# Optimization experiments

Hardware: AMD Instinct MI355X
Metric: run time of the kernel (lower is better)

## Reference

```python
import jax, jax.numpy as jnp
import numpy as np

UNITS = 128
INPUT_DIM = 784
OUTPUT_DIM = 10
NUM_LAYERS = 8
BATCH = 2048
DT = 0.1
EPS = 0.01
TOL = 1e-4
STEPS = 15


def setup_inputs() -> dict:
    key = jax.random.key(0)
    k = jax.random.split(key, 7)
    s_in = 1.0 / np.sqrt(INPUT_DIM)
    s_u = 1.0 / np.sqrt(UNITS)
    return {
        "x": jax.random.normal(k[0], (BATCH, INPUT_DIM), jnp.float32),
        "w_in": jax.random.uniform(k[1], (UNITS, INPUT_DIM), jnp.float32, -s_in, s_in),
        "b_in": jax.random.uniform(k[2], (UNITS,), jnp.float32, -s_in, s_in),
        "w_blocks": jax.random.uniform(k[3], (NUM_LAYERS, UNITS, UNITS), jnp.float32, -s_u, s_u),
        "b_blocks": jax.random.uniform(k[4], (NUM_LAYERS, UNITS), jnp.float32, -s_u, s_u),
        "w_out": jax.random.uniform(k[5], (OUTPUT_DIM, UNITS), jnp.float32, -s_u, s_u),
        "b_out": jax.random.uniform(k[6], (OUTPUT_DIM,), jnp.float32, -s_u, s_u),
    }


def _build_A(w_blocks):
    # A_l = [[I, dt*W_l], [-dt*W_l^T, (1+dt/eps)*I]], shape [L, 2u, 2u]
    I = jnp.broadcast_to(jnp.eye(UNITS, dtype=w_blocks.dtype), (NUM_LAYERS, UNITS, UNITS))
    top = jnp.concatenate([I, DT * w_blocks], axis=2)
    bot = jnp.concatenate([-DT * jnp.transpose(w_blocks, (0, 2, 1)), (1.0 + DT / EPS) * I], axis=2)
    return jnp.concatenate([top, bot], axis=1)


def _sweep(z_in, A, b_blocks):
    # Fixed-point sweeping (no-grad region in the original). z_ls: [L, B, 2u]
    B = z_in.shape[0]

    def layer_step(z, xs):
        A_l, b_l, z_l = xs
        rhs = jnp.concatenate(
            [jnp.broadcast_to(DT * b_l, (B, UNITS)), (DT / EPS) * jnp.tanh(z_l[:, :UNITS])],
            axis=1,
        ) + z
        # A_l is shared across the batch: one LU, many rhs
        y = jnp.linalg.solve(A_l, rhs.T).T
        err = jnp.mean(jnp.linalg.norm(z_l - y, axis=1))
        return y, (y, err)

    def body(state):
        z_ls, _, step = state
        _, (new_zls, errs) = jax.lax.scan(layer_step, z_in, (A, b_blocks, z_ls))
        return (new_zls, jnp.mean(errs), step + 1)

    def cond(state):
        _, err, step = state
        return jnp.logical_and(step < STEPS, err > TOL)

    z0 = jnp.broadcast_to(z_in[None], (NUM_LAYERS,) + z_in.shape)
    z_ls, _, _ = jax.lax.while_loop(cond, body, (z0, jnp.float32(10.0), jnp.int32(0)))
    return z_ls


def _block(z_in, W, b, z_l):
    # implicit_forward of one TransNetLayerSweeping (z_l is the converged sweep state)
    u_l, v_l = z_l[:, :UNITS], z_l[:, UNITS:]
    u_out = -DT * (v_l @ W.T) + z_in[:, :UNITS] + DT * b
    v_out = DT * (u_l @ W) + z_in[:, UNITS:] - (DT / EPS) * (v_l - jnp.tanh(u_l))
    return jnp.concatenate([u_out, v_out], axis=1)


def reference(x, w_in, b_in, w_blocks, b_blocks, w_out, b_out):
    x1 = x @ w_in.T + b_in                                  # [B, u]
    z_in = jnp.concatenate([x1, jnp.tanh(x1)], axis=1)      # [B, 2u]
    z_ls = _sweep(z_in, _build_A(w_blocks), b_blocks)       # [L, B, 2u]
    # Original loop does z = block.implicit_forward(z_in) for every block,
    # so only the LAST block's output survives.
    z_out = _block(z_in, w_blocks[-1], b_blocks[-1], z_ls[-1])
    logits = z_out[:, :UNITS] @ w_out.T + b_out             # [B, out]
    return jax.nn.softmax(logits, axis=1)
```

## Files before the change

### kernel.cpp

```cpp
#include <hip/hip_runtime.h>

#define U 128
#define BATCH 2048
#define NL 8
#define NS 8
#define DTc 0.1f
#define TENf 10.0f
#define INVC (1.0f/11.0f)
#define AFACT (0.01f/11.0f)
#define AST 264

typedef unsigned short u16;
typedef __attribute__((ext_vector_type(8))) short bf16x8;
typedef __attribute__((ext_vector_type(4))) float f32x4;
#define MFMA16(a,b,c) __builtin_amdgcn_mfma_f32_16x16x32_bf16(a,b,c,0,0,0)

__device__ __forceinline__ float bf2f(u16 h){ return __uint_as_float(((unsigned int)h)<<16); }
__device__ __forceinline__ u16 f2bf(float f){
  unsigned int u = __float_as_uint(f);
  u += 0x7FFFu + ((u >> 16) & 1u);
  return (u16)(u >> 16);
}
__device__ __forceinline__ float fast_tanh(float x){
  float e = __expf(2.0f*x);
  return 1.0f - __fdividef(2.0f, e + 1.0f);
}
__device__ __forceinline__ int detect_md(const u16* x, int* s_bad, int t, int nthr){
  if(t==0) *s_bad = 0;
  __syncthreads();
  int f=0;
  for(int i=t;i<4096;i+=nthr){ float v = bf2f(x[i]); if(!(fabsf(v)<16.0f)) f=1; }
  if(f) atomicOr(s_bad,1);
  __syncthreads();
  return *s_bad ? 0 : 1;
}

__global__ __launch_bounds__(256) void convK(
    const void* __restrict__ xraw, const void* __restrict__ w_in,
    const void* __restrict__ b_in, const void* __restrict__ wb,
    const void* __restrict__ bb, const void* __restrict__ w_out,
    const void* __restrict__ b_out,
    u16* __restrict__ winb, u16* __restrict__ Wg, u16* __restrict__ Wtg,
    float* __restrict__ bbD, float* __restrict__ b_in_f,
    float* __restrict__ w_out_f, float* __restrict__ b_out_f){
  __shared__ int s_bad;
  const int t = threadIdx.x;
  const int md = detect_md((const u16*)xraw, &s_bad, t, 256);
  const int g = blockIdx.x*256 + t, GS = gridDim.x*256;
  for(int i=g;i<100352;i+=GS) winb[i] = md ? ((const u16*)w_in)[i] : f2bf(((const float*)w_in)[i]);
  for(int i=g;i<131072;i+=GS){
    u16 h = md ? ((const u16*)wb)[i] : f2bf(((const float*)wb)[i]);
    Wg[i] = h;
    int L = i>>14, j = i & 16383;
    Wtg[(L<<14) + (j&127)*U + (j>>7)] = h;
  }
  for(int i=g;i<NL*U;i+=GS) bbD[i] = DTc * (md ? bf2f(((const u16*)bb)[i]) : ((const float*)bb)[i]);
  for(int i=g;i<U;i+=GS)    b_in_f[i]  = md ? bf2f(((const u16*)b_in)[i])  : ((const float*)b_in)[i];
  for(int i=g;i<1280;i+=GS) w_out_f[i] = md ? bf2f(((const u16*)w_out)[i]) : ((const float*)w_out)[i];
  for(int i=g;i<10;i+=GS)   b_out_f[i] = md ? bf2f(((const u16*)b_out)[i]) : ((const float*)b_out)[i];
}

template<typename EPI>
__device__ __forceinline__ void tile16(const u16* __restrict__ A, int lda,
                                       const u16* __restrict__ B, int ldb, EPI epi){
  const int lane = threadIdx.x & 63, w = threadIdx.x >> 6;
  const int ln = lane & 15, lq = lane >> 4;
  const int n0 = 32*w + ln, n1 = n0 + 16;
  bf16x8 af[4], b0[4], b1[4];
  #pragma unroll
  for(int kt=0;kt<4;kt++){
    af[kt] = *(const bf16x8*)&A[ln*lda + kt*32 + lq*8];
    b0[kt] = *(const bf16x8*)&B[n0*ldb + kt*32 + lq*8];
    b1[kt] = *(const bf16x8*)&B[n1*ldb + kt*32 + lq*8];
  }
  f32x4 a0 = {0,0,0,0}, a1 = {0,0,0,0};
  #pragma unroll
  for(int kt=0;kt<4;kt++){ a0 = MFMA16(af[kt], b0[kt], a0); a1 = MFMA16(af[kt], b1[kt], a1); }
  epi(a0, a1, n0, n1);
}

__global__ __launch_bounds__(256) void gemmP(const u16* __restrict__ Wtg, u16* __restrict__ Pg){
  const int L = blockIdx.x >> 3, mt = blockIdx.x & 7;
  const int lq = (threadIdx.x & 63) >> 4;
  const u16* WtL = Wtg + (L<<14);
  tile16(WtL + mt*16*U, U, WtL, U, [&](f32x4 a0, f32x4 a1, int n0, int n1){
    #pragma unroll
    for(int r=0;r<4;r++){
      int row = mt*16 + lq*4 + r;
      Pg[(L<<14) + row*U + n0] = f2bf(AFACT*a0[r]);
      Pg[(L<<14) + row*U + n1] = f2bf(AFACT*a1[r]);
    }
  });
}
__global__ __launch_bounds__(256) void gemmS(const u16* __restrict__ Pg, u16* __restrict__ Fb){
  const int L = blockIdx.x >> 3, mt = blockIdx.x & 7;
  const int lq = (threadIdx.x & 63) >> 4;
  const u16* PL = Pg + (L<<14);
  u16* FbL = Fb + (size_t)L*65536;
  tile16(PL + mt*16*U, U, PL, U, [&](f32x4 a0, f32x4 a1, int n0, int n1){
    #pragma unroll
    for(int r=0;r<4;r++){
      int row = mt*16 + lq*4 + r;
      FbL[row*256 + n0] = f2bf(INVC*(((row==n0)?1.0f:0.0f) - bf2f(PL[row*U+n0]) + a0[r]));
      FbL[row*256 + n1] = f2bf(INVC*(((row==n1)?1.0f:0.0f) - bf2f(PL[row*U+n1]) + a1[r]));
    }
  });
}
__global__ __launch_bounds__(256) void gemmQ(const u16* __restrict__ Fb, const u16* __restrict__ Wg,
                                             u16* __restrict__ FbW){
  const int L = blockIdx.x >> 3, mt = blockIdx.x & 7;
  const int lq = (threadIdx.x & 63) >> 4;
  const u16* FbL = Fb + (size_t)L*65536;
  u16* FbO = FbW + (size_t)L*65536;
  tile16(FbL + mt*16*256, 256, Wg + (L<<14), U, [&](f32x4 a0, f32x4 a1, int n0, int n1){
    #pragma unroll
    for(int r=0;r<4;r++){
      int row = mt*16 + lq*4 + r;
      u16 q0 = f2bf(DTc*a0[r]), q1 = f2bf(DTc*a1[r]);
      FbO[row*256 + 128 + n0] = q0;
      FbO[row*256 + 128 + n1] = q1;
      FbO[(128+n0)*256 + row] = q0;
      FbO[(128+n1)*256 + row] = q1;
    }
  });
}
__global__ __launch_bounds__(256) void gemmR(const u16* __restrict__ Wg, u16* __restrict__ Fb){
  const int L = blockIdx.x >> 3, mt = blockIdx.x & 7;
  const int lq = (threadIdx.x & 63) >> 4;
  u16* FbL = Fb + (size_t)L*65536;
  tile16(Wg + (L<<14) + mt*16*U, U, FbL + 128*256, 256, [&](f32x4 a0, f32x4 a1, int n0, int n1){
    #pragma unroll
    for(int r=0;r<4;r++){
      int row = mt*16 + lq*4 + r;
      FbL[(128+row)*256 + 128 + n0] = f2bf(DTc*a0[r]);
      FbL[(128+row)*256 + 128 + n1] = f2bf(DTc*a1[r]);
    }
  });
}
__global__ __launch_bounds__(256) void swizK(const u16* __restrict__ Fb, u16* __restrict__ Fsw){
  const int L = blockIdx.x >> 3, part = blockIdx.x & 7;
  const u16* FbL = Fb + (size_t)L*65536;
  for(int i = part*1024 + threadIdx.x; i < (part+1)*1024; i += 256){
    int lanei = i & 63, kt = (i>>6)&7, c = (i>>9)&3, w = (i>>11)&3;
    int lni = lanei & 15, lqi = lanei >> 4;
    int row_n = 64*w + 16*c + lni;
    int col_k = kt*32 + lqi*8;
    *(bf16x8*)&Fsw[((size_t)L*8192 + i)*8] = *(const bf16x8*)&FbL[row_n*256 + col_k];
  }
}

__global__ __launch_bounds__(512,1) void mainK(
    const void* __restrict__ xraw, const u16* __restrict__ winb,
    const float* __restrict__ b_in_f, const bf16x8* __restrict__ Fsw,
    const float* __restrict__ bbD, const float* __restrict__ w_out_f,
    const float* __restrict__ b_out_f, void* __restrict__ outraw){
  __shared__ u16 At[2][16*AST];
  __shared__ unsigned zh32[NL][16][64];
  __shared__ float zinu[16*U];
  __shared__ float bbL[NL*U];
  __shared__ float lg[16*12];
  __shared__ int s_bad;
  float* uout = (float*)&At[0][0];

  const int t = threadIdx.x;
  const int lane = t & 63, wid = t >> 6, ln = lane & 15, lq = lane >> 4;
  const int r0 = blockIdx.x * 16;

  const int md = detect_md((const u16*)xraw, &s_bad, t, 512);
  for(int i=t;i<NL*U;i+=512) bbL[i] = bbD[i];
  __syncthreads();

  {
    const int n0 = 16*wid + ln;
    f32x4 acc = {0,0,0,0};
    for(int kt=0; kt<25; ++kt){
      int k0 = kt*32 + lq*8;
      bf16x8 av = {0,0,0,0,0,0,0,0}, bv = {0,0,0,0,0,0,0,0};
      if(k0 < 784){
        if(md){
          av = *(const bf16x8*)((const u16*)xraw + (size_t)(r0+ln)*784 + k0);
        } else {
          const float* xp = (const float*)xraw + (size_t)(r0+ln)*784 + k0;
          float4 f0 = *(const float4*)xp, f1 = *(const float4*)(xp+4);
          av[0]=(short)f2bf(f0.x); av[1]=(short)f2bf(f0.y); av[2]=(short)f2bf(f0.z); av[3]=(short)f2bf(f0.w);
          av[4]=(short)f2bf(f1.x); av[5]=(short)f2bf(f1.y); av[6]=(short)f2bf(f1.z); av[7]=(short)f2bf(f1.w);
        }
        bv = *(const bf16x8*)&winb[(size_t)n0*784 + k0];
      }
      acc = MFMA16(av, bv, acc);
    }
    #pragma unroll
    for(int r=0;r<4;r++) zinu[(lq*4+r)*U + n0] = acc[r] + b_in_f[n0];
  }
  __syncthreads();

  for(int i=t; i<NL*16*64; i+=512){
    int l = i>>10, row = (i>>6)&15, p = i & 63;
    int lo = 32*(p>>4) + (p&15);
    zh32[l][row][p] = ((unsigned)f2bf(zinu[row*U + lo + 16]) << 16) | f2bf(zinu[row*U + lo]);
  }
  float ru[2][4];
  if(wid < 4){
    #pragma unroll
    for(int cc=0;cc<2;cc++){
      int n = 32*wid + 16*cc + ln;
      #pragma unroll
      for(int r=0;r<4;r++){
        int row = lq*4 + r;
        At[0][row*AST + n] = f2bf((TENf + 1.0f) * fast_tanh(zinu[row*U + n]));
      }
    }
  } else {
    int w4 = wid - 4;
    #pragma unroll
    for(int cc=0;cc<2;cc++){
      int uc = 32*w4 + 16*cc + ln;
      #pragma unroll
      for(int r=0;r<4;r++){
        int row = lq*4 + r;
        float v = zinu[row*U + uc] + bbL[uc];
        ru[cc][r] = v;
        At[0][row*AST + 128 + uc] = f2bf(v);
      }
    }
  }
  const bf16x8* fbase = Fsw + (wid>>1)*2048 + (wid&1)*1024 + lane;
  bf16x8 BfA[2][8], BfB[2][8];
  #pragma unroll
  for(int cc=0;cc<2;cc++){
    #pragma unroll
    for(int kt=0;kt<8;kt++) BfA[cc][kt] = fbase[cc*512 + kt*64];
  }
  __syncthreads();

#define STEPBODY(STEPV, BC, BN, CURC) { \
    const int l = (STEPV) & 7; \
    const int lnext = (l+1) & 7; \
    const bool last = ((STEPV) == NS*NL-1); \
    { const bf16x8* fp = fbase + lnext*8192; \
      _Pragma("unroll") \
      for(int cc=0;cc<2;cc++){ _Pragma("unroll") for(int kt=0;kt<8;kt++) BN[cc][kt] = fp[cc*512 + kt*64]; } } \
    bf16x8 at8[8]; \
    _Pragma("unroll") \
    for(int kt=0;kt<8;kt++) at8[kt] = *(const bf16x8*)&At[CURC][ln*AST + kt*32 + lq*8]; \
    float th[2][4]; \
    if(wid < 4 && !last){ \
      _Pragma("unroll") \
      for(int r=0;r<4;r++){ \
        unsigned pk = zh32[lnext][lq*4 + r][16*wid + ln]; \
        th[0][r] = TENf * fast_tanh(bf2f((u16)(pk & 0xffff))); \
        th[1][r] = TENf * fast_tanh(bf2f((u16)(pk >> 16))); \
      } \
    } \
    f32x4 acc[2] = {{0,0,0,0},{0,0,0,0}}; \
    _Pragma("unroll") \
    for(int kt=0;kt<8;kt++){ \
      acc[0] = MFMA16(at8[kt], BC[0][kt], acc[0]); \
      acc[1] = MFMA16(at8[kt], BC[1][kt], acc[1]); \
    } \
    if(wid < 4){ \
      if(!last){ \
        const bool wrap = (l == 7); \
        _Pragma("unroll") \
        for(int cc=0;cc<2;cc++){ \
          int n = 32*wid + 16*cc + ln; \
          _Pragma("unroll") \
          for(int r=0;r<4;r++){ \
            int row = lq*4 + r; \
            float base = wrap ? fast_tanh(zinu[row*U + n]) : acc[cc][r]; \
            At[1-(CURC)][row*AST + n] = f2bf(th[cc][r] + base); \
          } \
        } \
      } \
    } else { \
      int w4 = wid - 4; \
      _Pragma("unroll") \
      for(int r=0;r<4;r++){ \
        int row = lq*4 + r; \
        int uc0 = 32*w4 + ln; \
        float yu0 = ru[0][r] - acc[0][r]; \
        float yu1 = ru[1][r] - acc[1][r]; \
        zh32[l][row][16*w4 + ln] = ((unsigned)f2bf(yu1)<<16) | f2bf(yu0); \
        if(last){ \
          uout[row*U + uc0]      = zinu[row*U + uc0]      + bbL[7*U + uc0]      - acc[0][r]; \
          uout[row*U + uc0 + 16] = zinu[row*U + uc0 + 16] + bbL[7*U + uc0 + 16] - acc[1][r]; \
        } else if(l == 7){ \
          float rn0 = zinu[row*U + uc0]      + bbL[uc0]; \
          float rn1 = zinu[row*U + uc0 + 16] + bbL[uc0 + 16]; \
          ru[0][r] = rn0; ru[1][r] = rn1; \
          At[1-(CURC)][row*AST + 128 + uc0]      = f2bf(rn0); \
          At[1-(CURC)][row*AST + 128 + uc0 + 16] = f2bf(rn1); \
        } else { \
          float rn0 = yu0 + bbL[(l+1)*U + uc0]; \
          float rn1 = yu1 + bbL[(l+1)*U + uc0 + 16]; \
          ru[0][r] = rn0; ru[1][r] = rn1; \
          At[1-(CURC)][row*AST + 128 + uc0]      = f2bf(rn0); \
          At[1-(CURC)][row*AST + 128 + uc0 + 16] = f2bf(rn1); \
        } \
      } \
    } \
    __syncthreads(); \
  }

  for(int sp=0; sp<NS*NL; sp+=2){
    STEPBODY(sp,   BfA, BfB, 0)
    STEPBODY(sp+1, BfB, BfA, 1)
  }
#undef STEPBODY

  if(t < 160){
    int mm = t/10, o = t - mm*10;
    float a = b_out_f[o];
    const float* wo = w_out_f + o*U;
    for(int k=0;k<U;k++) a += uout[mm*U + k]*wo[k];
    lg[mm*12 + o] = a;
  }
  __syncthreads();
  if(t < 16){
    float mx = -1e30f;
    for(int o=0;o<10;o++) mx = fmaxf(mx, lg[t*12 + o]);
    float e[10]; float sum = 0.0f;
    for(int o=0;o<10;o++){ e[o] = __expf(lg[t*12 + o] - mx); sum += e[o]; }
    float inv = 1.0f / sum;
    for(int o=0;o<10;o++){
      float pv = e[o]*inv;
      if(md) ((u16*)outraw)[(size_t)(r0 + t)*10 + o] = f2bf(pv);
      else   ((float*)outraw)[(size_t)(r0 + t)*10 + o] = pv;
    }
  }
}

extern "C" void kernel_launch(void* const* d_in, const int* in_sizes, int n_in,
                              void* d_out, int out_size, void* d_ws, size_t ws_size,
                              hipStream_t stream) {
  char* p = (char*)d_ws;
  u16* Fb      = (u16*)p;  p += (size_t)8*256*256*2;
  u16* Fsw     = (u16*)p;  p += (size_t)8*256*256*2;
  u16* Wg      = (u16*)p;  p += (size_t)8*128*128*2;
  u16* Wtg     = (u16*)p;  p += (size_t)8*128*128*2;
  u16* Pg      = (u16*)p;  p += (size_t)8*128*128*2;
  u16* winb    = (u16*)p;  p += 200704;
  float* bbD   = (float*)p; p += 4096;
  float* b_in_f = (float*)p; p += 512;
  float* w_out_f = (float*)p; p += 5120;
  float* b_out_f = (float*)p; p += 64;

  convK<<<128, 256, 0, stream>>>(d_in[0], d_in[1], d_in[2], d_in[3], d_in[4],
                                 d_in[5], d_in[6],
                                 winb, Wg, Wtg, bbD, b_in_f, w_out_f, b_out_f);
  gemmP<<<64, 256, 0, stream>>>(Wtg, Pg);
  gemmS<<<64, 256, 0, stream>>>(Pg, Fb);
  gemmQ<<<64, 256, 0, stream>>>(Fb, Wg, Fb);
  gemmR<<<64, 256, 0, stream>>>(Wg, Fb);
  swizK<<<64, 256, 0, stream>>>(Fb, Fsw);
  mainK<<<BATCH/16, 512, 0, stream>>>(d_in[0], winb, b_in_f, (const bf16x8*)Fsw, bbD,
                                      w_out_f, b_out_f, d_out);
}
```

Before: 206.6 us.

## Fuse weight-prep kernels into one per-layer kernel and read raw inputs in main kernel

The six preprocessing launches (conversion, three-stage Neumann-style GEMM chain, swizzle) are merged into a single kernel with one 512-thread block per layer that runs the chain with block-level barriers. The main kernel now reads w_in, biases and output weights straight from the raw inputs, converting to bf16 on the fly, which removes the conversion pass and its workspace traffic. The input projection loop is also unrolled with the tail K-chunk handled separately. Shared-memory padding is added to zh32 to avoid bank conflicts, and the per-step barrier is replaced with an explicit lgkmcnt wait plus s_barrier. The cost is only 8 blocks doing the prep work serially, and repeated fp32 to bf16 conversion of w_in in every main block.

```diff
diff --git a/kernel.cpp b/kernel.cpp
--- a/kernel.cpp
+++ b/kernel.cpp
@@ -34,113 +34,86 @@
   __syncthreads();
   return *s_bad ? 0 : 1;
 }
-
-__global__ __launch_bounds__(256) void convK(
-    const void* __restrict__ xraw, const void* __restrict__ w_in,
-    const void* __restrict__ b_in, const void* __restrict__ wb,
-    const void* __restrict__ bb, const void* __restrict__ w_out,
-    const void* __restrict__ b_out,
-    u16* __restrict__ winb, u16* __restrict__ Wg, u16* __restrict__ Wtg,
-    float* __restrict__ bbD, float* __restrict__ b_in_f,
-    float* __restrict__ w_out_f, float* __restrict__ b_out_f){
+__device__ __forceinline__ bf16x8 ld8f(const float* p){
+  float4 f0 = *(const float4*)p, f1 = *(const float4*)(p+4);
+  bf16x8 v;
+  v[0]=(short)f2bf(f0.x); v[1]=(short)f2bf(f0.y); v[2]=(short)f2bf(f0.z); v[3]=(short)f2bf(f0.w);
+  v[4]=(short)f2bf(f1.x); v[5]=(short)f2bf(f1.y); v[6]=(short)f2bf(f1.z); v[7]=(short)f2bf(f1.w);
+  return v;
+}
+__device__ __forceinline__ void lgkm_barrier(){
+  __builtin_amdgcn_sched_barrier(0);
+  asm volatile("s_waitcnt lgkmcnt(0)\n\ts_barrier" ::: "memory");
+  __builtin_amdgcn_sched_barrier(0);
+}
+
+template<typename EPI>
+__device__ __forceinline__ void g128(const u16* __restrict__ A, int lda,
+                                     const u16* __restrict__ B, int ldb, EPI epi){
+  const int lane = threadIdx.x & 63, wid = threadIdx.x >> 6;
+  const int ln = lane & 15, lq = lane >> 4;
+  bf16x8 af[4];
+  #pragma unroll
+  for(int kt=0;kt<4;kt++) af[kt] = *(const bf16x8*)&A[(wid*16+ln)*lda + kt*32 + lq*8];
+  #pragma unroll
+  for(int c=0;c<8;c++){
+    const int n0 = c*16 + ln;
+    f32x4 acc = {0,0,0,0};
+    #pragma unroll
+    for(int kt=0;kt<4;kt++)
+      acc = MFMA16(af[kt], *(const bf16x8*)&B[n0*ldb + kt*32 + lq*8], acc);
+    epi(acc, wid*16 + lq*4, n0);
+  }
+}
+
+__global__ __launch_bounds__(512) void prepF(
+    const void* __restrict__ xraw, const void* __restrict__ wb,
+    u16* __restrict__ Wg, u16* __restrict__ Wtg, u16* __restrict__ Pg,
+    u16* __restrict__ Fb, u16* __restrict__ Fsw){
   __shared__ int s_bad;
-  const int t = threadIdx.x;
-  const int md = detect_md((const u16*)xraw, &s_bad, t, 256);
-  const int g = blockIdx.x*256 + t, GS = gridDim.x*256;
-  for(int i=g;i<100352;i+=GS) winb[i] = md ? ((const u16*)w_in)[i] : f2bf(((const float*)w_in)[i]);
-  for(int i=g;i<131072;i+=GS){
-    u16 h = md ? ((const u16*)wb)[i] : f2bf(((const float*)wb)[i]);
-    Wg[i] = h;
-    int L = i>>14, j = i & 16383;
-    Wtg[(L<<14) + (j&127)*U + (j>>7)] = h;
-  }
-  for(int i=g;i<NL*U;i+=GS) bbD[i] = DTc * (md ? bf2f(((const u16*)bb)[i]) : ((const float*)bb)[i]);
-  for(int i=g;i<U;i+=GS)    b_in_f[i]  = md ? bf2f(((const u16*)b_in)[i])  : ((const float*)b_in)[i];
-  for(int i=g;i<1280;i+=GS) w_out_f[i] = md ? bf2f(((const u16*)w_out)[i]) : ((const float*)w_out)[i];
-  for(int i=g;i<10;i+=GS)   b_out_f[i] = md ? bf2f(((const u16*)b_out)[i]) : ((const float*)b_out)[i];
-}
-
-template<typename EPI>
-__device__ __forceinline__ void tile16(const u16* __restrict__ A, int lda,
-                                       const u16* __restrict__ B, int ldb, EPI epi){
-  const int lane = threadIdx.x & 63, w = threadIdx.x >> 6;
-  const int ln = lane & 15, lq = lane >> 4;
-  const int n0 = 32*w + ln, n1 = n0 + 16;
-  bf16x8 af[4], b0[4], b1[4];
-  #pragma unroll
-  for(int kt=0;kt<4;kt++){
-    af[kt] = *(const bf16x8*)&A[ln*lda + kt*32 + lq*8];
-    b0[kt] = *(const bf16x8*)&B[n0*ldb + kt*32 + lq*8];
-    b1[kt] = *(const bf16x8*)&B[n1*ldb + kt*32 + lq*8];
-  }
-  f32x4 a0 = {0,0,0,0}, a1 = {0,0,0,0};
-  #pragma unroll
-  for(int kt=0;kt<4;kt++){ a0 = MFMA16(af[kt], b0[kt], a0); a1 = MFMA16(af[kt], b1[kt], a1); }
-  epi(a0, a1, n0, n1);
-}
-
-__global__ __launch_bounds__(256) void gemmP(const u16* __restrict__ Wtg, u16* __restrict__ Pg){
-  const int L = blockIdx.x >> 3, mt = blockIdx.x & 7;
-  const int lq = (threadIdx.x & 63) >> 4;
-  const u16* WtL = Wtg + (L<<14);
-  tile16(WtL + mt*16*U, U, WtL, U, [&](f32x4 a0, f32x4 a1, int n0, int n1){
+  const int t = threadIdx.x, L = blockIdx.x;
+  const int md = detect_md((const u16*)xraw, &s_bad, t, 512);
+  u16* WgL = Wg  + (L<<14);
+  u16* WtL = Wtg + (L<<14);
+  u16* PL  = Pg  + (L<<14);
+  u16* FbL = Fb  + (size_t)L*65536;
+
+  for(int j=t;j<16384;j+=512){
+    u16 h = md ? ((const u16*)wb)[(L<<14)+j] : f2bf(((const float*)wb)[(L<<14)+j]);
+    WgL[j] = h;
+    WtL[(j&127)*U + (j>>7)] = h;
+  }
+  __syncthreads();
+  g128(WtL, U, WtL, U, [&](f32x4 acc, int rowb, int n0){
+    #pragma unroll
+    for(int r=0;r<4;r++) PL[(rowb+r)*U + n0] = f2bf(AFACT*acc[r]);
+  });
+  __syncthreads();
+  g128(PL, U, PL, U, [&](f32x4 acc, int rowb, int n0){
     #pragma unroll
     for(int r=0;r<4;r++){
-      int row = mt*16 + lq*4 + r;
-      Pg[(L<<14) + row*U + n0] = f2bf(AFACT*a0[r]);
-      Pg[(L<<14) + row*U + n1] = f2bf(AFACT*a1[r]);
+      int row = rowb + r;
+      FbL[row*256 + n0] = f2bf(INVC*(((row==n0)?1.0f:0.0f) - bf2f(PL[row*U+n0]) + acc[r]));
     }
   });
-}
-__global__ __launch_bounds__(256) void gemmS(const u16* __restrict__ Pg, u16* __restrict__ Fb){
-  const int L = blockIdx.x >> 3, mt = blockIdx.x & 7;
-  const int lq = (threadIdx.x & 63) >> 4;
-  const u16* PL = Pg + (L<<14);
-  u16* FbL = Fb + (size_t)L*65536;
-  tile16(PL + mt*16*U, U, PL, U, [&](f32x4 a0, f32x4 a1, int n0, int n1){
+  __syncthreads();
+  g128(FbL, 256, WgL, U, [&](f32x4 acc, int rowb, int n0){
     #pragma unroll
     for(int r=0;r<4;r++){
-      int row = mt*16 + lq*4 + r;
-      FbL[row*256 + n0] = f2bf(INVC*(((row==n0)?1.0f:0.0f) - bf2f(PL[row*U+n0]) + a0[r]));
-      FbL[row*256 + n1] = f2bf(INVC*(((row==n1)?1.0f:0.0f) - bf2f(PL[row*U+n1]) + a1[r]));
+      int row = rowb + r;
+      u16 q = f2bf(DTc*acc[r]);
+      FbL[row*256 + 128 + n0] = q;
+      FbL[(128+n0)*256 + row] = q;
     }
   });
-}
-__global__ __launch_bounds__(256) void gemmQ(const u16* __restrict__ Fb, const u16* __restrict__ Wg,
-                                             u16* __restrict__ FbW){
-  const int L = blockIdx.x >> 3, mt = blockIdx.x & 7;
-  const int lq = (threadIdx.x & 63) >> 4;
-  const u16* FbL = Fb + (size_t)L*65536;
-  u16* FbO = FbW + (size_t)L*65536;
-  tile16(FbL + mt*16*256, 256, Wg + (L<<14), U, [&](f32x4 a0, f32x4 a1, int n0, int n1){
-    #pragma unroll
-    for(int r=0;r<4;r++){
-      int row = mt*16 + lq*4 + r;
-      u16 q0 = f2bf(DTc*a0[r]), q1 = f2bf(DTc*a1[r]);
-      FbO[row*256 + 128 + n0] = q0;
-      FbO[row*256 + 128 + n1] = q1;
-      FbO[(128+n0)*256 + row] = q0;
-      FbO[(128+n1)*256 + row] = q1;
-    }
+  __syncthreads();
+  g128(WgL, U, FbL + 128*256, 256, [&](f32x4 acc, int rowb, int n0){
+    #pragma unroll
+    for(int r=0;r<4;r++)
+      FbL[(128+rowb+r)*256 + 128 + n0] = f2bf(DTc*acc[r]);
   });
-}
-__global__ __launch_bounds__(256) void gemmR(const u16* __restrict__ Wg, u16* __restrict__ Fb){
-  const int L = blockIdx.x >> 3, mt = blockIdx.x & 7;
-  const int lq = (threadIdx.x & 63) >> 4;
-  u16* FbL = Fb + (size_t)L*65536;
-  tile16(Wg + (L<<14) + mt*16*U, U, FbL + 128*256, 256, [&](f32x4 a0, f32x4 a1, int n0, int n1){
-    #pragma unroll
-    for(int r=0;r<4;r++){
-      int row = mt*16 + lq*4 + r;
-      FbL[(128+row)*256 + 128 + n0] = f2bf(DTc*a0[r]);
-      FbL[(128+row)*256 + 128 + n1] = f2bf(DTc*a1[r]);
-    }
-  });
-}
-__global__ __launch_bounds__(256) void swizK(const u16* __restrict__ Fb, u16* __restrict__ Fsw){
-  const int L = blockIdx.x >> 3, part = blockIdx.x & 7;
-  const u16* FbL = Fb + (size_t)L*65536;
-  for(int i = part*1024 + threadIdx.x; i < (part+1)*1024; i += 256){
+  __syncthreads();
+  for(int i=t;i<8192;i+=512){
     int lanei = i & 63, kt = (i>>6)&7, c = (i>>9)&3, w = (i>>11)&3;
     int lni = lanei & 15, lqi = lanei >> 4;
     int row_n = 64*w + 16*c + lni;
@@ -150,12 +123,12 @@
 }
 
 __global__ __launch_bounds__(512,1) void mainK(
-    const void* __restrict__ xraw, const u16* __restrict__ winb,
-    const float* __restrict__ b_in_f, const bf16x8* __restrict__ Fsw,
-    const float* __restrict__ bbD, const float* __restrict__ w_out_f,
-    const float* __restrict__ b_out_f, void* __restrict__ outraw){
+    const void* __restrict__ xraw, const void* __restrict__ w_in,
+    const void* __restrict__ b_in, const void* __restrict__ bb,
+    const bf16x8* __restrict__ Fsw, const void* __restrict__ w_out,
+    const void* __restrict__ b_out, void* __restrict__ outraw){
   __shared__ u16 At[2][16*AST];
-  __shared__ unsigned zh32[NL][16][64];
+  __shared__ unsigned zh32[NL][16][66];
   __shared__ float zinu[16*U];
   __shared__ float bbL[NL*U];
   __shared__ float lg[16*12];
@@ -167,30 +140,44 @@
   const int r0 = blockIdx.x * 16;
 
   const int md = detect_md((const u16*)xraw, &s_bad, t, 512);
-  for(int i=t;i<NL*U;i+=512) bbL[i] = bbD[i];
+  for(int i=t;i<NL*U;i+=512)
+    bbL[i] = DTc * (md ? bf2f(((const u16*)bb)[i]) : ((const float*)bb)[i]);
   __syncthreads();
 
   {
     const int n0 = 16*wid + ln;
+    const u16*   wrb = (const u16*)w_in   + (size_t)n0*784;
+    const float* wrf = (const float*)w_in + (size_t)n0*784;
+    const u16*   xrb = (const u16*)xraw   + (size_t)(r0+ln)*784;
+    const float* xrf = (const float*)xraw + (size_t)(r0+ln)*784;
     f32x4 acc = {0,0,0,0};
-    for(int kt=0; kt<25; ++kt){
-      int k0 = kt*32 + lq*8;
-      bf16x8 av = {0,0,0,0,0,0,0,0}, bv = {0,0,0,0,0,0,0,0};
-      if(k0 < 784){
-        if(md){
-          av = *(const bf16x8*)((const u16*)xraw + (size_t)(r0+ln)*784 + k0);
-        } else {
-          const float* xp = (const float*)xraw + (size_t)(r0+ln)*784 + k0;
-          float4 f0 = *(const float4*)xp, f1 = *(const float4*)(xp+4);
-          av[0]=(short)f2bf(f0.x); av[1]=(short)f2bf(f0.y); av[2]=(short)f2bf(f0.z); av[3]=(short)f2bf(f0.w);
-          av[4]=(short)f2bf(f1.x); av[5]=(short)f2bf(f1.y); av[6]=(short)f2bf(f1.z); av[7]=(short)f2bf(f1.w);
-        }
-        bv = *(const bf16x8*)&winb[(size_t)n0*784 + k0];
-      }
-      acc = MFMA16(av, bv, acc);
-    }
-    #pragma unroll
-    for(int r=0;r<4;r++) zinu[(lq*4+r)*U + n0] = acc[r] + b_in_f[n0];
+    const bf16x8 z8 = {0,0,0,0,0,0,0,0};
+    if(md){
+      #pragma unroll
+      for(int kt=0; kt<24; ++kt){
+        int k0 = kt*32 + lq*8;
+        acc = MFMA16(*(const bf16x8*)(xrb + k0), *(const bf16x8*)(wrb + k0), acc);
+      }
+      { int k0 = 768 + lq*8;
+        bf16x8 av = z8, bv = z8;
+        if(lq < 2){ av = *(const bf16x8*)(xrb + k0); bv = *(const bf16x8*)(wrb + k0); }
+        acc = MFMA16(av, bv, acc);
+      }
+    } else {
+      #pragma unroll 4
+      for(int kt=0; kt<24; ++kt){
+        int k0 = kt*32 + lq*8;
+        acc = MFMA16(ld8f(xrf + k0), ld8f(wrf + k0), acc);
+      }
+      { int k0 = 768 + lq*8;
+        bf16x8 av = z8, bv = z8;
+        if(lq < 2){ av = ld8f(xrf + k0); bv = ld8f(wrf + k0); }
+        acc = MFMA16(av, bv, acc);
+      }
+    }
+    float bi = md ? bf2f(((const u16*)b_in)[n0]) : ((const float*)b_in)[n0];
+    #pragma unroll
+    for(int r=0;r<4;r++) zinu[(lq*4+r)*U + n0] = acc[r] + bi;
   }
   __syncthreads();
 
@@ -299,7 +286,7 @@
         } \
       } \
     } \
-    __syncthreads(); \
+    lgkm_barrier(); \
   }
 
   for(int sp=0; sp<NS*NL; sp+=2){
@@ -310,9 +297,14 @@
 
   if(t < 160){
     int mm = t/10, o = t - mm*10;
-    float a = b_out_f[o];
-    const float* wo = w_out_f + o*U;
-    for(int k=0;k<U;k++) a += uout[mm*U + k]*wo[k];
+    float a = md ? bf2f(((const u16*)b_out)[o]) : ((const float*)b_out)[o];
+    if(md){
+      const u16* wo = (const u16*)w_out + o*U;
+      for(int k=0;k<U;k++) a += uout[mm*U + k]*bf2f(wo[k]);
+    } else {
+      const float* wo = (const float*)w_out + o*U;
+      for(int k=0;k<U;k++) a += uout[mm*U + k]*wo[k];
+    }
     lg[mm*12 + o] = a;
   }
   __syncthreads();
@@ -339,20 +331,8 @@
   u16* Wg      = (u16*)p;  p += (size_t)8*128*128*2;
   u16* Wtg     = (u16*)p;  p += (size_t)8*128*128*2;
   u16* Pg      = (u16*)p;  p += (size_t)8*128*128*2;
-  u16* winb    = (u16*)p;  p += 200704;
-  float* bbD   = (float*)p; p += 4096;
-  float* b_in_f = (float*)p; p += 512;
-  float* w_out_f = (float*)p; p += 5120;
-  float* b_out_f = (float*)p; p += 64;
-
-  convK<<<128, 256, 0, stream>>>(d_in[0], d_in[1], d_in[2], d_in[3], d_in[4],
-                                 d_in[5], d_in[6],
-                                 winb, Wg, Wtg, bbD, b_in_f, w_out_f, b_out_f);
-  gemmP<<<64, 256, 0, stream>>>(Wtg, Pg);
-  gemmS<<<64, 256, 0, stream>>>(Pg, Fb);
-  gemmQ<<<64, 256, 0, stream>>>(Fb, Wg, Fb);
-  gemmR<<<64, 256, 0, stream>>>(Wg, Fb);
-  swizK<<<64, 256, 0, stream>>>(Fb, Fsw);
-  mainK<<<BATCH/16, 512, 0, stream>>>(d_in[0], winb, b_in_f, (const bf16x8*)Fsw, bbD,
-                                      w_out_f, b_out_f, d_out);
-}
+
+  prepF<<<8, 512, 0, stream>>>(d_in[0], d_in[3], Wg, Wtg, Pg, Fb, Fsw);
+  mainK<<<BATCH/16, 512, 0, stream>>>(d_in[0], d_in[1], d_in[2], d_in[4],
+                                      (const bf16x8*)Fsw, d_in[5], d_in[6], d_out);
+}
```

Measured after the change: 245.4 us. 18.8% more time.

## Double mainK workgroup to 1024 threads and fold weight conversions into it

Applied to the files above, without the earlier changes.

The main sweep kernel moves from 512 to 1024 threads per block. Each wave now computes one 16-column MFMA tile instead of two, which halves the per-wave register footprint and the serial MFMA chain per step. The input-projection, bias and output-layer conversions are removed from convK and done inline in mainK from the raw inputs, so the bf16 copy of w_in no longer takes a separate pass. The per-step __syncthreads is replaced by an explicit lgkmcnt wait plus s_barrier, and the tanh state buffer changes to an unpacked bf16 layout. The risks are more barrier participants per step and every block converting fp32 weights redundantly.

```diff
diff --git a/kernel.cpp b/kernel.cpp
--- a/kernel.cpp
+++ b/kernel.cpp
@@ -34,30 +34,32 @@
   __syncthreads();
   return *s_bad ? 0 : 1;
 }
+__device__ __forceinline__ bf16x8 ld8f(const float* p){
+  float4 f0 = *(const float4*)p, f1 = *(const float4*)(p+4);
+  bf16x8 v;
+  v[0]=(short)f2bf(f0.x); v[1]=(short)f2bf(f0.y); v[2]=(short)f2bf(f0.z); v[3]=(short)f2bf(f0.w);
+  v[4]=(short)f2bf(f1.x); v[5]=(short)f2bf(f1.y); v[6]=(short)f2bf(f1.z); v[7]=(short)f2bf(f1.w);
+  return v;
+}
+__device__ __forceinline__ void lgkm_barrier(){
+  __builtin_amdgcn_sched_barrier(0);
+  asm volatile("s_waitcnt lgkmcnt(0)\n\ts_barrier" ::: "memory");
+  __builtin_amdgcn_sched_barrier(0);
+}
 
 __global__ __launch_bounds__(256) void convK(
-    const void* __restrict__ xraw, const void* __restrict__ w_in,
-    const void* __restrict__ b_in, const void* __restrict__ wb,
-    const void* __restrict__ bb, const void* __restrict__ w_out,
-    const void* __restrict__ b_out,
-    u16* __restrict__ winb, u16* __restrict__ Wg, u16* __restrict__ Wtg,
-    float* __restrict__ bbD, float* __restrict__ b_in_f,
-    float* __restrict__ w_out_f, float* __restrict__ b_out_f){
+    const void* __restrict__ xraw, const void* __restrict__ wb,
+    u16* __restrict__ Wg, u16* __restrict__ Wtg){
   __shared__ int s_bad;
   const int t = threadIdx.x;
   const int md = detect_md((const u16*)xraw, &s_bad, t, 256);
   const int g = blockIdx.x*256 + t, GS = gridDim.x*256;
-  for(int i=g;i<100352;i+=GS) winb[i] = md ? ((const u16*)w_in)[i] : f2bf(((const float*)w_in)[i]);
   for(int i=g;i<131072;i+=GS){
     u16 h = md ? ((const u16*)wb)[i] : f2bf(((const float*)wb)[i]);
     Wg[i] = h;
     int L = i>>14, j = i & 16383;
     Wtg[(L<<14) + (j&127)*U + (j>>7)] = h;
   }
-  for(int i=g;i<NL*U;i+=GS) bbD[i] = DTc * (md ? bf2f(((const u16*)bb)[i]) : ((const float*)bb)[i]);
-  for(int i=g;i<U;i+=GS)    b_in_f[i]  = md ? bf2f(((const u16*)b_in)[i])  : ((const float*)b_in)[i];
-  for(int i=g;i<1280;i+=GS) w_out_f[i] = md ? bf2f(((const u16*)w_out)[i]) : ((const float*)w_out)[i];
-  for(int i=g;i<10;i+=GS)   b_out_f[i] = md ? bf2f(((const u16*)b_out)[i]) : ((const float*)b_out)[i];
 }
 
 template<typename EPI>
@@ -149,13 +151,13 @@
   }
 }
 
-__global__ __launch_bounds__(512,1) void mainK(
-    const void* __restrict__ xraw, const u16* __restrict__ winb,
-    const float* __restrict__ b_in_f, const bf16x8* __restrict__ Fsw,
-    const float* __restrict__ bbD, const float* __restrict__ w_out_f,
-    const float* __restrict__ b_out_f, void* __restrict__ outraw){
+__global__ __launch_bounds__(1024,1) void mainK(
+    const void* __restrict__ xraw, const void* __restrict__ w_in,
+    const void* __restrict__ b_in, const void* __restrict__ bb,
+    const bf16x8* __restrict__ Fsw, const void* __restrict__ w_out,
+    const void* __restrict__ b_out, void* __restrict__ outraw){
   __shared__ u16 At[2][16*AST];
-  __shared__ unsigned zh32[NL][16][64];
+  __shared__ u16 zh16[NL][16][132];
   __shared__ float zinu[16*U];
   __shared__ float bbL[NL*U];
   __shared__ float lg[16*12];
@@ -166,71 +168,74 @@
   const int lane = t & 63, wid = t >> 6, ln = lane & 15, lq = lane >> 4;
   const int r0 = blockIdx.x * 16;
 
-  const int md = detect_md((const u16*)xraw, &s_bad, t, 512);
-  for(int i=t;i<NL*U;i+=512) bbL[i] = bbD[i];
-  __syncthreads();
-
-  {
+  const int md = detect_md((const u16*)xraw, &s_bad, t, 1024);
+  for(int i=t;i<NL*U;i+=1024)
+    bbL[i] = DTc * (md ? bf2f(((const u16*)bb)[i]) : ((const float*)bb)[i]);
+  __syncthreads();
+
+  if(wid < 8){
     const int n0 = 16*wid + ln;
+    const u16*   wrb = (const u16*)w_in   + (size_t)n0*784;
+    const float* wrf = (const float*)w_in + (size_t)n0*784;
+    const u16*   xrb = (const u16*)xraw   + (size_t)(r0+ln)*784;
+    const float* xrf = (const float*)xraw + (size_t)(r0+ln)*784;
     f32x4 acc = {0,0,0,0};
-    for(int kt=0; kt<25; ++kt){
-      int k0 = kt*32 + lq*8;
-      bf16x8 av = {0,0,0,0,0,0,0,0}, bv = {0,0,0,0,0,0,0,0};
-      if(k0 < 784){
-        if(md){
-          av = *(const bf16x8*)((const u16*)xraw + (size_t)(r0+ln)*784 + k0);
-        } else {
-          const float* xp = (const float*)xraw + (size_t)(r0+ln)*784 + k0;
-          float4 f0 = *(const float4*)xp, f1 = *(const float4*)(xp+4);
-          av[0]=(short)f2bf(f0.x); av[1]=(short)f2bf(f0.y); av[2]=(short)f2bf(f0.z); av[3]=(short)f2bf(f0.w);
-          av[4]=(short)f2bf(f1.x); av[5]=(short)f2bf(f1.y); av[6]=(short)f2bf(f1.z); av[7]=(short)f2bf(f1.w);
-        }
-        bv = *(const bf16x8*)&winb[(size_t)n0*784 + k0];
+    const bf16x8 z8 = {0,0,0,0,0,0,0,0};
+    if(md){
+      #pragma unroll
+      for(int kt=0; kt<24; ++kt){
+        int k0 = kt*32 + lq*8;
+        acc = MFMA16(*(const bf16x8*)(xrb + k0), *(const bf16x8*)(wrb + k0), acc);
       }
-      acc = MFMA16(av, bv, acc);
-    }
-    #pragma unroll
-    for(int r=0;r<4;r++) zinu[(lq*4+r)*U + n0] = acc[r] + b_in_f[n0];
-  }
-  __syncthreads();
-
-  for(int i=t; i<NL*16*64; i+=512){
-    int l = i>>10, row = (i>>6)&15, p = i & 63;
-    int lo = 32*(p>>4) + (p&15);
-    zh32[l][row][p] = ((unsigned)f2bf(zinu[row*U + lo + 16]) << 16) | f2bf(zinu[row*U + lo]);
-  }
-  float ru[2][4];
-  if(wid < 4){
-    #pragma unroll
-    for(int cc=0;cc<2;cc++){
-      int n = 32*wid + 16*cc + ln;
-      #pragma unroll
-      for(int r=0;r<4;r++){
-        int row = lq*4 + r;
-        At[0][row*AST + n] = f2bf((TENf + 1.0f) * fast_tanh(zinu[row*U + n]));
+      { int k0 = 768 + lq*8;
+        bf16x8 av = z8, bv = z8;
+        if(lq < 2){ av = *(const bf16x8*)(xrb + k0); bv = *(const bf16x8*)(wrb + k0); }
+        acc = MFMA16(av, bv, acc);
       }
+    } else {
+      #pragma unroll 4
+      for(int kt=0; kt<24; ++kt){
+        int k0 = kt*32 + lq*8;
+        acc = MFMA16(ld8f(xrf + k0), ld8f(wrf + k0), acc);
+      }
+      { int k0 = 768 + lq*8;
+        bf16x8 av = z8, bv = z8;
+        if(lq < 2){ av = ld8f(xrf + k0); bv = ld8f(wrf + k0); }
+        acc = MFMA16(av, bv, acc);
+      }
+    }
+    float bi = md ? bf2f(((const u16*)b_in)[n0]) : ((const float*)b_in)[n0];
+    #pragma unroll
+    for(int r=0;r<4;r++) zinu[(lq*4+r)*U + n0] = acc[r] + bi;
+  }
+  __syncthreads();
+
+  for(int i=t; i<NL*16*128; i+=1024){
+    int l = i>>11, row = (i>>7)&15, c = i & 127;
+    zh16[l][row][c] = f2bf(zinu[row*U + c]);
+  }
+  float ru[4];
+  if(wid < 8){
+    const int n = 16*wid + ln;
+    #pragma unroll
+    for(int r=0;r<4;r++){
+      int row = lq*4 + r;
+      At[0][row*AST + n] = f2bf((TENf + 1.0f) * fast_tanh(zinu[row*U + n]));
     }
   } else {
-    int w4 = wid - 4;
-    #pragma unroll
-    for(int cc=0;cc<2;cc++){
-      int uc = 32*w4 + 16*cc + ln;
-      #pragma unroll
-      for(int r=0;r<4;r++){
-        int row = lq*4 + r;
-        float v = zinu[row*U + uc] + bbL[uc];
-        ru[cc][r] = v;
-        At[0][row*AST + 128 + uc] = f2bf(v);
-      }
-    }
-  }
-  const bf16x8* fbase = Fsw + (wid>>1)*2048 + (wid&1)*1024 + lane;
-  bf16x8 BfA[2][8], BfB[2][8];
+    const int uc = 16*(wid-8) + ln;
+    #pragma unroll
+    for(int r=0;r<4;r++){
+      int row = lq*4 + r;
+      float v = zinu[row*U + uc] + bbL[uc];
+      ru[r] = v;
+      At[0][row*AST + 128 + uc] = f2bf(v);
+    }
+  }
+  const bf16x8* fbase = Fsw + (wid>>2)*2048 + (wid&3)*512 + lane;
+  bf16x8 BfA[8], BfB[8];
   #pragma unroll
-  for(int cc=0;cc<2;cc++){
-    #pragma unroll
-    for(int kt=0;kt<8;kt++) BfA[cc][kt] = fbase[cc*512 + kt*64];
-  }
+  for(int kt=0;kt<8;kt++) BfA[kt] = fbase[kt*64];
   __syncthreads();
 
 #define STEPBODY(STEPV, BC, BN, CURC) { \
@@ -239,67 +244,50 @@
     const bool last = ((STEPV) == NS*NL-1); \
     { const bf16x8* fp = fbase + lnext*8192; \
       _Pragma("unroll") \
-      for(int cc=0;cc<2;cc++){ _Pragma("unroll") for(int kt=0;kt<8;kt++) BN[cc][kt] = fp[cc*512 + kt*64]; } } \
+      for(int kt=0;kt<8;kt++) BN[kt] = fp[kt*64]; } \
     bf16x8 at8[8]; \
     _Pragma("unroll") \
     for(int kt=0;kt<8;kt++) at8[kt] = *(const bf16x8*)&At[CURC][ln*AST + kt*32 + lq*8]; \
-    float th[2][4]; \
-    if(wid < 4 && !last){ \
+    float th[4]; \
+    if(wid < 8 && !last){ \
       _Pragma("unroll") \
-      for(int r=0;r<4;r++){ \
-        unsigned pk = zh32[lnext][lq*4 + r][16*wid + ln]; \
-        th[0][r] = TENf * fast_tanh(bf2f((u16)(pk & 0xffff))); \
-        th[1][r] = TENf * fast_tanh(bf2f((u16)(pk >> 16))); \
-      } \
+      for(int r=0;r<4;r++) th[r] = TENf * fast_tanh(bf2f(zh16[lnext][lq*4 + r][16*wid + ln])); \
     } \
-    f32x4 acc[2] = {{0,0,0,0},{0,0,0,0}}; \
+    f32x4 acc = {0,0,0,0}; \
     _Pragma("unroll") \
-    for(int kt=0;kt<8;kt++){ \
-      acc[0] = MFMA16(at8[kt], BC[0][kt], acc[0]); \
-      acc[1] = MFMA16(at8[kt], BC[1][kt], acc[1]); \
-    } \
-    if(wid < 4){ \
+    for(int kt=0;kt<8;kt++) acc = MFMA16(at8[kt], BC[kt], acc); \
+    if(wid < 8){ \
       if(!last){ \
         const bool wrap = (l == 7); \
+        const int n = 16*wid + ln; \
         _Pragma("unroll") \
-        for(int cc=0;cc<2;cc++){ \
-          int n = 32*wid + 16*cc + ln; \
-          _Pragma("unroll") \
-          for(int r=0;r<4;r++){ \
-            int row = lq*4 + r; \
-            float base = wrap ? fast_tanh(zinu[row*U + n]) : acc[cc][r]; \
-            At[1-(CURC)][row*AST + n] = f2bf(th[cc][r] + base); \
-          } \
+        for(int r=0;r<4;r++){ \
+          int row = lq*4 + r; \
+          float base = wrap ? fast_tanh(zinu[row*U + n]) : acc[r]; \
+          At[1-(CURC)][row*AST + n] = f2bf(th[r] + base); \
         } \
       } \
     } else { \
-      int w4 = wid - 4; \
+      const int uc0 = 16*(wid-8) + ln; \
       _Pragma("unroll") \
       for(int r=0;r<4;r++){ \
         int row = lq*4 + r; \
-        int uc0 = 32*w4 + ln; \
-        float yu0 = ru[0][r] - acc[0][r]; \
-        float yu1 = ru[1][r] - acc[1][r]; \
-        zh32[l][row][16*w4 + ln] = ((unsigned)f2bf(yu1)<<16) | f2bf(yu0); \
+        float yu = ru[r] - acc[r]; \
+        zh16[l][row][uc0] = f2bf(yu); \
         if(last){ \
-          uout[row*U + uc0]      = zinu[row*U + uc0]      + bbL[7*U + uc0]      - acc[0][r]; \
-          uout[row*U + uc0 + 16] = zinu[row*U + uc0 + 16] + bbL[7*U + uc0 + 16] - acc[1][r]; \
+          uout[row*U + uc0] = zinu[row*U + uc0] + bbL[7*U + uc0] - acc[r]; \
         } else if(l == 7){ \
-          float rn0 = zinu[row*U + uc0]      + bbL[uc0]; \
-          float rn1 = zinu[row*U + uc0 + 16] + bbL[uc0 + 16]; \
-          ru[0][r] = rn0; ru[1][r] = rn1; \
-          At[1-(CURC)][row*AST + 128 + uc0]      = f2bf(rn0); \
-          At[1-(CURC)][row*AST + 128 + uc0 + 16] = f2bf(rn1); \
+          float rn = zinu[row*U + uc0] + bbL[uc0]; \
+          ru[r] = rn; \
+          At[1-(CURC)][row*AST + 128 + uc0] = f2bf(rn); \
         } else { \
-          float rn0 = yu0 + bbL[(l+1)*U + uc0]; \
-          float rn1 = yu1 + bbL[(l+1)*U + uc0 + 16]; \
-          ru[0][r] = rn0; ru[1][r] = rn1; \
-          At[1-(CURC)][row*AST + 128 + uc0]      = f2bf(rn0); \
-          At[1-(CURC)][row*AST + 128 + uc0 + 16] = f2bf(rn1); \
+          float rn = yu + bbL[(l+1)*U + uc0]; \
+          ru[r] = rn; \
+          At[1-(CURC)][row*AST + 128 + uc0] = f2bf(rn); \
         } \
       } \
     } \
-    __syncthreads(); \
+    lgkm_barrier(); \
   }
 
   for(int sp=0; sp<NS*NL; sp+=2){
@@ -310,9 +298,14 @@
 
   if(t < 160){
     int mm = t/10, o = t - mm*10;
-    float a = b_out_f[o];
-    const float* wo = w_out_f + o*U;
-    for(int k=0;k<U;k++) a += uout[mm*U + k]*wo[k];
+    float a = md ? bf2f(((const u16*)b_out)[o]) : ((const float*)b_out)[o];
+    if(md){
+      const u16* wo = (const u16*)w_out + o*U;
+      for(int k=0;k<U;k++) a += uout[mm*U + k]*bf2f(wo[k]);
+    } else {
+      const float* wo = (const float*)w_out + o*U;
+      for(int k=0;k<U;k++) a += uout[mm*U + k]*wo[k];
+    }
     lg[mm*12 + o] = a;
   }
   __syncthreads();
@@ -339,20 +332,13 @@
   u16* Wg      = (u16*)p;  p += (size_t)8*128*128*2;
   u16* Wtg     = (u16*)p;  p += (size_t)8*128*128*2;
   u16* Pg      = (u16*)p;  p += (size_t)8*128*128*2;
-  u16* winb    = (u16*)p;  p += 200704;
-  float* bbD   = (float*)p; p += 4096;
-  float* b_in_f = (float*)p; p += 512;
-  float* w_out_f = (float*)p; p += 5120;
-  float* b_out_f = (float*)p; p += 64;
-
-  convK<<<128, 256, 0, stream>>>(d_in[0], d_in[1], d_in[2], d_in[3], d_in[4],
-                                 d_in[5], d_in[6],
-                                 winb, Wg, Wtg, bbD, b_in_f, w_out_f, b_out_f);
+
+  convK<<<128, 256, 0, stream>>>(d_in[0], d_in[3], Wg, Wtg);
   gemmP<<<64, 256, 0, stream>>>(Wtg, Pg);
   gemmS<<<64, 256, 0, stream>>>(Pg, Fb);
   gemmQ<<<64, 256, 0, stream>>>(Fb, Wg, Fb);
   gemmR<<<64, 256, 0, stream>>>(Wg, Fb);
   swizK<<<64, 256, 0, stream>>>(Fb, Fsw);
-  mainK<<<BATCH/16, 512, 0, stream>>>(d_in[0], winb, b_in_f, (const bf16x8*)Fsw, bbD,
-                                      w_out_f, b_out_f, d_out);
-}
+  mainK<<<BATCH/16, 1024, 0, stream>>>(d_in[0], d_in[1], d_in[2], d_in[4],
+                                       (const bf16x8*)Fsw, d_in[5], d_in[6], d_out);
+}
```

New measurement: 203.2 us. Within noise of the previous version (-1.6%).
